# Optimization experiments

Hardware: AMD Instinct MI355X
Metric: run time of the kernel (lower is better)

The kernel has to match this reference:

```python
import jax, jax.numpy as jnp
import numpy as np

EMBED = 8   # forced: combine_heads Linear(embed_dim, embed_dim) applied to 8-wire measurement
FFN = 32
B, S = 128, 8192
EPS = 1e-5


def _layernorm(x, g, b):
    m = x.mean(-1, keepdims=True)
    v = ((x - m) ** 2).mean(-1, keepdims=True)
    return (x - m) * jax.lax.rsqrt(v + EPS) * g + b


def setup_inputs() -> dict:
    key = jax.random.key(0)
    ks = jax.random.split(key, 8)

    def lin(k, fi, fo):
        return jax.random.normal(k, (fi, fo), jnp.float32) / np.sqrt(fi).astype(np.float32)

    return dict(
        x=jax.random.normal(ks[0], (B, S, EMBED), jnp.float32),
        Wq=lin(ks[1], EMBED, EMBED), bq=jnp.zeros((EMBED,), jnp.float32),
        theta_attn=jax.random.uniform(ks[2], (EMBED,), jnp.float32, -np.pi, np.pi),
        Wc=lin(ks[3], EMBED, EMBED), bc=jnp.zeros((EMBED,), jnp.float32),
        g1=jnp.ones((EMBED,), jnp.float32), beta1=jnp.zeros((EMBED,), jnp.float32),
        theta_ffn=jax.random.uniform(ks[4], (EMBED,), jnp.float32, -np.pi, np.pi),
        W1=lin(ks[5], EMBED, FFN), b1=jnp.zeros((FFN,), jnp.float32),
        W2=lin(ks[6], FFN, EMBED), b2=jnp.zeros((EMBED,), jnp.float32),
        g2=jnp.ones((EMBED,), jnp.float32), beta2=jnp.zeros((EMBED,), jnp.float32),
    )


def reference(x, Wq, bq, theta_attn, Wc, bc, g1, beta1,
              theta_ffn, W1, b1, W2, b2, g2, beta2):
    # --- MultiHeadAttentionQuantum (eval mode, dropout = identity) ---
    # q_linear; the 8-wire encoder consumes all 8 features of q per token.
    q = x @ Wq + bq                           # [B, S, 8]
    # Circuit per token: RX(q_i) then trainable RX(theta_i) on wire i -> RX(q_i+theta_i),
    # then CNOT ring (0->1,...,6->7, 7->0), then <Z_i>.
    # All-RX product state => basis probs p_i(1)=sin^2(a_i/2); CNOTs permute basis
    # states (prefix-XOR of bits), so analytically:
    #   <Z_k> = prod_{j=0..k} cos(a_j)  for k>=1;   <Z_0> = prod_{j=1..7} cos(a_j)
    ca = jnp.cos(q + theta_attn)              # [B, S, 8]
    z_rest = jnp.cumprod(ca, axis=-1)[..., 1:]
    z0 = jnp.prod(ca[..., 1:], axis=-1, keepdims=True)
    z = jnp.concatenate([z0, z_rest], axis=-1)
    attn_out = z @ Wc + bc                    # combine_heads

    x1 = _layernorm(x + attn_out, g1, beta1)

    # --- FeedForwardQuantum: RX(x_i) then RY(theta_i), no entanglers ->
    #     <Z_i> = cos(theta_i) * cos(x_i)  (product state, per-wire closed form)
    zf = jnp.cos(theta_ffn) * jnp.cos(x1)     # [B, S, 8]
    h = jax.nn.relu(zf @ W1 + b1)             # linear1 -> relu
    ffn_out = h @ W2 + b2                     # linear2

    return _layernorm(x1 + ffn_out, g2, beta2)
```

## Files before the change

kernel.cpp:

```cpp
#include <hip/hip_runtime.h>


#define NTOK   (128 * 8192)
#define T      2
#define NTHREADS 256
#define NBLOCKS  (NTOK / (T * NTHREADS))
#define TSTRIDE  (NTOK / T)
#define LN_EPS 1e-5f

__device__ __forceinline__ float fast_cos(float x) {
    return __builtin_amdgcn_cosf(x * 0.15915494309189535f);
}

__global__ __launch_bounds__(NTHREADS, 6)
void qtb_kernel(const float* __restrict__ x,
                const float* __restrict__ Wq,  const float* __restrict__ bq,
                const float* __restrict__ tha,
                const float* __restrict__ Wc,  const float* __restrict__ bc,
                const float* __restrict__ g1,  const float* __restrict__ be1,
                const float* __restrict__ thf,
                const float* __restrict__ W1,  const float* __restrict__ b1,
                const float* __restrict__ W2,  const float* __restrict__ b2,
                const float* __restrict__ g2,  const float* __restrict__ be2,
                float* __restrict__ out)
{
    const int g = blockIdx.x * NTHREADS + threadIdx.x;

    float xv[T][8];
#pragma unroll
    for (int t = 0; t < T; ++t) {
        const float4* p = reinterpret_cast<const float4*>(x) + (size_t)(t * TSTRIDE + g) * 2;
        float4 a = p[0];
        float4 b = p[1];
        xv[t][0] = a.x; xv[t][1] = a.y; xv[t][2] = a.z; xv[t][3] = a.w;
        xv[t][4] = b.x; xv[t][5] = b.y; xv[t][6] = b.z; xv[t][7] = b.w;
    }

    float attn[T][8];
#pragma unroll
    for (int t = 0; t < T; ++t)
#pragma unroll
        for (int j = 0; j < 8; ++j) attn[t][j] = bc[j];

    float cp[T];
    float cp1[T];
#pragma unroll
    for (int k = 0; k < 8; ++k) {
        const float bqk = bq[k];
        const float thk = tha[k];
        float wq[8], wc[8];
#pragma unroll
        for (int i = 0; i < 8; ++i) wq[i] = Wq[i * 8 + k];
#pragma unroll
        for (int j = 0; j < 8; ++j) wc[j] = Wc[k * 8 + j];
#pragma unroll
        for (int t = 0; t < T; ++t) {
            float q = bqk;
#pragma unroll
            for (int i = 0; i < 8; ++i) q += xv[t][i] * wq[i];
            float ca = fast_cos(q + thk);
            if (k == 0) {
                cp[t] = ca;
                cp1[t] = 1.0f;
            } else {
                cp[t]  *= ca;
                cp1[t] *= ca;
#pragma unroll
                for (int j = 0; j < 8; ++j) attn[t][j] += cp[t] * wc[j];
            }
        }
    }
    {
        float wc0[8];
#pragma unroll
        for (int j = 0; j < 8; ++j) wc0[j] = Wc[j];
#pragma unroll
        for (int t = 0; t < T; ++t)
#pragma unroll
            for (int j = 0; j < 8; ++j) attn[t][j] += cp1[t] * wc0[j];
    }

    float cf[8];
#pragma unroll
    for (int j = 0; j < 8; ++j) cf[j] = fast_cos(thf[j]);
    float sg1[8], sb1[8];
#pragma unroll
    for (int j = 0; j < 8; ++j) { sg1[j] = g1[j]; sb1[j] = be1[j]; }

    float zf[T][8];
#pragma unroll
    for (int t = 0; t < T; ++t) {
        float y[8];
        float s = 0.f;
#pragma unroll
        for (int j = 0; j < 8; ++j) { y[j] = xv[t][j] + attn[t][j]; s += y[j]; }
        float m = s * 0.125f;
        float v = 0.f;
#pragma unroll
        for (int j = 0; j < 8; ++j) { float d = y[j] - m; v += d * d; }
        float r = rsqrtf(v * 0.125f + LN_EPS);
#pragma unroll
        for (int j = 0; j < 8; ++j) {
            float x1 = (y[j] - m) * r * sg1[j] + sb1[j];
            xv[t][j] = x1;
            zf[t][j] = cf[j] * fast_cos(x1);
        }
    }

    float ffn[T][8];
    {
        float sb2[8];
#pragma unroll
        for (int j = 0; j < 8; ++j) sb2[j] = b2[j];
#pragma unroll
        for (int t = 0; t < T; ++t)
#pragma unroll
            for (int j = 0; j < 8; ++j) ffn[t][j] = sb2[j];
    }
#pragma unroll
    for (int m = 0; m < 32; ++m) {
        const float b1m = b1[m];
        float w1[8], w2[8];
#pragma unroll
        for (int i = 0; i < 8; ++i) w1[i] = W1[i * 32 + m];
#pragma unroll
        for (int j = 0; j < 8; ++j) w2[j] = W2[m * 8 + j];
#pragma unroll
        for (int t = 0; t < T; ++t) {
            float h = b1m;
#pragma unroll
            for (int i = 0; i < 8; ++i) h += zf[t][i] * w1[i];
            h = fmaxf(h, 0.f);
#pragma unroll
            for (int j = 0; j < 8; ++j) ffn[t][j] += h * w2[j];
        }
    }

    float sg2[8], sbb2[8];
#pragma unroll
    for (int j = 0; j < 8; ++j) { sg2[j] = g2[j]; sbb2[j] = be2[j]; }
#pragma unroll
    for (int t = 0; t < T; ++t) {
        float y[8];
        float s = 0.f;
#pragma unroll
        for (int j = 0; j < 8; ++j) { y[j] = xv[t][j] + ffn[t][j]; s += y[j]; }
        float m = s * 0.125f;
        float v = 0.f;
#pragma unroll
        for (int j = 0; j < 8; ++j) { float d = y[j] - m; v += d * d; }
        float r = rsqrtf(v * 0.125f + LN_EPS);
        float o[8];
#pragma unroll
        for (int j = 0; j < 8; ++j) o[j] = (y[j] - m) * r * sg2[j] + sbb2[j];
        float4* q = reinterpret_cast<float4*>(out) + (size_t)(t * TSTRIDE + g) * 2;
        q[0] = make_float4(o[0], o[1], o[2], o[3]);
        q[1] = make_float4(o[4], o[5], o[6], o[7]);
    }
}

extern "C" void kernel_launch(void* const* d_in, const int* in_sizes, int n_in,
                              void* d_out, int out_size, void* d_ws, size_t ws_size,
                              hipStream_t stream) {
    (void)in_sizes; (void)n_in; (void)d_ws; (void)ws_size; (void)out_size;
    qtb_kernel<<<NBLOCKS, NTHREADS, 0, stream>>>(
        (const float*)d_in[0],
        (const float*)d_in[1],
        (const float*)d_in[2],
        (const float*)d_in[3],
        (const float*)d_in[4],
        (const float*)d_in[5],
        (const float*)d_in[6],
        (const float*)d_in[7],
        (const float*)d_in[8],
        (const float*)d_in[9],
        (const float*)d_in[10],
        (const float*)d_in[11],
        (const float*)d_in[12],
        (const float*)d_in[13],
        (const float*)d_in[14],
        (float*)d_out);
}
```

Before: 137.4 us.

## Use packed fp16 dot2 for q projection and FFN matmuls with prepacked weights

Adds a small pre-kernel that packs Wq, W1 and W2 into half2 pairs in the workspace. The main kernel converts x, the FFN cos features and the hidden activations to fp16 pairs and accumulates with v_dot2 into fp32, roughly halving the FMA count in the VALU-bound inner loops. The layernorm rsqrt now uses the raw hardware intrinsic. This lowers precision of the inputs to cos and the FFN, which can hurt accuracy, and adds an extra kernel launch per call.

```diff
diff --git a/kernel.cpp b/kernel.cpp
--- a/kernel.cpp
+++ b/kernel.cpp
@@ -8,25 +8,61 @@
 #define TSTRIDE  (NTOK / T)
 #define LN_EPS 1e-5f
 
+typedef __fp16 half2_t __attribute__((ext_vector_type(2)));
+
+union PK { unsigned u; half2_t h; };
+
 __device__ __forceinline__ float fast_cos(float x) {
     return __builtin_amdgcn_cosf(x * 0.15915494309189535f);
 }
+__device__ __forceinline__ float fast_rsqrt(float x) {
+    return __builtin_amdgcn_rsqf(x);
+}
+__device__ __forceinline__ unsigned packh2(float a, float b) {
+    PK c; c.h = __builtin_amdgcn_cvt_pkrtz(a, b); return c.u;
+}
+__device__ __forceinline__ float dot2(half2_t a, unsigned bw, float c) {
+    PK b; b.u = bw;
+    return __builtin_amdgcn_fdot2(a, b.h, c, false);
+}
+
+__global__ void pack_weights(const float* __restrict__ Wq,
+                             const float* __restrict__ W1,
+                             const float* __restrict__ W2,
+                             unsigned* __restrict__ ws)
+{
+    int idx = threadIdx.x;
+    if (idx < 32) {
+        int k = idx >> 2, p = idx & 3;
+        ws[idx] = packh2(Wq[(2 * p) * 8 + k], Wq[(2 * p + 1) * 8 + k]);
+    } else if (idx < 160) {
+        int i2 = idx - 32;
+        int m = i2 >> 2, p = i2 & 3;
+        ws[idx] = packh2(W1[(2 * p) * 32 + m], W1[(2 * p + 1) * 32 + m]);
+    } else if (idx < 288) {
+        int i2 = idx - 160;
+        int mp = i2 >> 3, j = i2 & 7;
+        ws[idx] = packh2(W2[(2 * mp) * 8 + j], W2[(2 * mp + 1) * 8 + j]);
+    }
+}
 
 __global__ __launch_bounds__(NTHREADS, 6)
 void qtb_kernel(const float* __restrict__ x,
-                const float* __restrict__ Wq,  const float* __restrict__ bq,
+                const float* __restrict__ bq,
                 const float* __restrict__ tha,
                 const float* __restrict__ Wc,  const float* __restrict__ bc,
                 const float* __restrict__ g1,  const float* __restrict__ be1,
                 const float* __restrict__ thf,
-                const float* __restrict__ W1,  const float* __restrict__ b1,
-                const float* __restrict__ W2,  const float* __restrict__ b2,
+                const float* __restrict__ b1,
+                const float* __restrict__ b2,
                 const float* __restrict__ g2,  const float* __restrict__ be2,
+                const unsigned* __restrict__ wp,
                 float* __restrict__ out)
 {
     const int g = blockIdx.x * NTHREADS + threadIdx.x;
 
     float xv[T][8];
+    half2_t xp[T][4];
 #pragma unroll
     for (int t = 0; t < T; ++t) {
         const float4* p = reinterpret_cast<const float4*>(x) + (size_t)(t * TSTRIDE + g) * 2;
@@ -34,6 +70,10 @@
         float4 b = p[1];
         xv[t][0] = a.x; xv[t][1] = a.y; xv[t][2] = a.z; xv[t][3] = a.w;
         xv[t][4] = b.x; xv[t][5] = b.y; xv[t][6] = b.z; xv[t][7] = b.w;
+        xp[t][0] = __builtin_amdgcn_cvt_pkrtz(a.x, a.y);
+        xp[t][1] = __builtin_amdgcn_cvt_pkrtz(a.z, a.w);
+        xp[t][2] = __builtin_amdgcn_cvt_pkrtz(b.x, b.y);
+        xp[t][3] = __builtin_amdgcn_cvt_pkrtz(b.z, b.w);
     }
 
     float attn[T][8];
@@ -48,16 +88,14 @@
     for (int k = 0; k < 8; ++k) {
         const float bqk = bq[k];
         const float thk = tha[k];
-        float wq[8], wc[8];
-#pragma unroll
-        for (int i = 0; i < 8; ++i) wq[i] = Wq[i * 8 + k];
+        float wc[8];
 #pragma unroll
         for (int j = 0; j < 8; ++j) wc[j] = Wc[k * 8 + j];
 #pragma unroll
         for (int t = 0; t < T; ++t) {
             float q = bqk;
 #pragma unroll
-            for (int i = 0; i < 8; ++i) q += xv[t][i] * wq[i];
+            for (int p = 0; p < 4; ++p) q = dot2(xp[t][p], wp[k * 4 + p], q);
             float ca = fast_cos(q + thk);
             if (k == 0) {
                 cp[t] = ca;
@@ -87,7 +125,7 @@
 #pragma unroll
     for (int j = 0; j < 8; ++j) { sg1[j] = g1[j]; sb1[j] = be1[j]; }
 
-    float zf[T][8];
+    half2_t zfp[T][4];
 #pragma unroll
     for (int t = 0; t < T; ++t) {
         float y[8];
@@ -98,13 +136,17 @@
         float v = 0.f;
 #pragma unroll
         for (int j = 0; j < 8; ++j) { float d = y[j] - m; v += d * d; }
-        float r = rsqrtf(v * 0.125f + LN_EPS);
+        float r = fast_rsqrt(v * 0.125f + LN_EPS);
+        float zf[8];
 #pragma unroll
         for (int j = 0; j < 8; ++j) {
             float x1 = (y[j] - m) * r * sg1[j] + sb1[j];
             xv[t][j] = x1;
-            zf[t][j] = cf[j] * fast_cos(x1);
+            zf[j] = cf[j] * fast_cos(x1);
         }
+#pragma unroll
+        for (int p = 0; p < 4; ++p)
+            zfp[t][p] = __builtin_amdgcn_cvt_pkrtz(zf[2 * p], zf[2 * p + 1]);
     }
 
     float ffn[T][8];
@@ -118,21 +160,26 @@
             for (int j = 0; j < 8; ++j) ffn[t][j] = sb2[j];
     }
 #pragma unroll
-    for (int m = 0; m < 32; ++m) {
-        const float b1m = b1[m];
-        float w1[8], w2[8];
-#pragma unroll
-        for (int i = 0; i < 8; ++i) w1[i] = W1[i * 32 + m];
-#pragma unroll
-        for (int j = 0; j < 8; ++j) w2[j] = W2[m * 8 + j];
+    for (int mp = 0; mp < 16; ++mp) {
+        const int m0 = 2 * mp, m1 = 2 * mp + 1;
+        const float b1a = b1[m0];
+        const float b1b = b1[m1];
+        unsigned w2p[8];
+#pragma unroll
+        for (int j = 0; j < 8; ++j) w2p[j] = wp[160 + mp * 8 + j];
 #pragma unroll
         for (int t = 0; t < T; ++t) {
-            float h = b1m;
-#pragma unroll
-            for (int i = 0; i < 8; ++i) h += zf[t][i] * w1[i];
-            h = fmaxf(h, 0.f);
-#pragma unroll
-            for (int j = 0; j < 8; ++j) ffn[t][j] += h * w2[j];
+            float h0 = b1a, h1 = b1b;
+#pragma unroll
+            for (int p = 0; p < 4; ++p) {
+                h0 = dot2(zfp[t][p], wp[32 + m0 * 4 + p], h0);
+                h1 = dot2(zfp[t][p], wp[32 + m1 * 4 + p], h1);
+            }
+            h0 = fmaxf(h0, 0.f);
+            h1 = fmaxf(h1, 0.f);
+            half2_t hp = __builtin_amdgcn_cvt_pkrtz(h0, h1);
+#pragma unroll
+            for (int j = 0; j < 8; ++j) ffn[t][j] = dot2(hp, w2p[j], ffn[t][j]);
         }
     }
 
@@ -149,7 +196,7 @@
         float v = 0.f;
 #pragma unroll
         for (int j = 0; j < 8; ++j) { float d = y[j] - m; v += d * d; }
-        float r = rsqrtf(v * 0.125f + LN_EPS);
+        float r = fast_rsqrt(v * 0.125f + LN_EPS);
         float o[8];
 #pragma unroll
         for (int j = 0; j < 8; ++j) o[j] = (y[j] - m) * r * sg2[j] + sbb2[j];
@@ -162,10 +209,15 @@
 extern "C" void kernel_launch(void* const* d_in, const int* in_sizes, int n_in,
                               void* d_out, int out_size, void* d_ws, size_t ws_size,
                               hipStream_t stream) {
-    (void)in_sizes; (void)n_in; (void)d_ws; (void)ws_size; (void)out_size;
+    (void)in_sizes; (void)n_in; (void)ws_size; (void)out_size;
+    unsigned* wp = (unsigned*)d_ws;
+    pack_weights<<<1, 320, 0, stream>>>(
+        (const float*)d_in[1],
+        (const float*)d_in[9],
+        (const float*)d_in[11],
+        wp);
     qtb_kernel<<<NBLOCKS, NTHREADS, 0, stream>>>(
         (const float*)d_in[0],
-        (const float*)d_in[1],
         (const float*)d_in[2],
         (const float*)d_in[3],
         (const float*)d_in[4],
@@ -173,11 +225,10 @@
         (const float*)d_in[6],
         (const float*)d_in[7],
         (const float*)d_in[8],
-        (const float*)d_in[9],
         (const float*)d_in[10],
-        (const float*)d_in[11],
         (const float*)d_in[12],
         (const float*)d_in[13],
         (const float*)d_in[14],
+        wp,
         (float*)d_out);
 }
```

Result: faster. 123.0 us (-10.5%).
